# Kernel tuning notes

Measured on AMD Instinct MI355X. Metric: run time of the kernel, lower is better.

Reference implementation:

```python
import jax, jax.numpy as jnp
import numpy as np

N_SRC = 50000
N_DST = 50000
N_EDGES = 800000
D = 128
H = 128


def setup_inputs() -> dict:
    key = jax.random.key(0)
    ks = jax.random.split(key, 10)
    return {
        "feat_src": jax.random.normal(ks[0], (N_SRC, D), dtype=jnp.float32),
        "feat_dst": jax.random.normal(ks[1], (N_DST, D), dtype=jnp.float32),
        "W1": jax.random.normal(ks[2], (H, D), dtype=jnp.float32) * 0.05,
        "b1": jnp.zeros((H,), dtype=jnp.float32),
        "W2": jax.random.normal(ks[3], (H, 3 * D), dtype=jnp.float32) * 0.05,
        "b2": jnp.zeros((H,), dtype=jnp.float32),
        "W3": jax.random.normal(ks[4], (H, 2 * H), dtype=jnp.float32) * 0.05,
        "b3": jnp.zeros((H,), dtype=jnp.float32),
        "src_idx": jax.random.randint(ks[5], (N_EDGES,), 0, N_SRC, dtype=jnp.int32),
        "dst_idx": jax.random.randint(ks[6], (N_EDGES,), 0, N_DST, dtype=jnp.int32),
    }


def reference(feat_src, feat_dst, W1, b1, W2, b2, W3, b3, src_idx, dst_idx):
    n_dst = feat_dst.shape[0]
    # copy_u: gather source features along edges  [E, D]
    m = feat_src[src_idx]
    # fn.max -> 'max'; NOTE: source code's 'mean' is ALSO fn.max (faithful to bug)
    mx = jax.ops.segment_max(m, dst_idx, num_segments=n_dst)
    mx = jnp.where(jnp.isfinite(mx), mx, jnp.zeros_like(mx))  # zero-degree dst -> 0 (DGL convention)
    sm = jax.ops.segment_sum(m, dst_idx, num_segments=n_dst)
    agg = jnp.concatenate([mx, mx, sm], axis=1)  # [N_dst, 3D]
    z2 = agg @ W2.T + b2            # fc2
    z1 = feat_dst @ W1.T + b1       # fc1
    h = jax.nn.relu(jnp.concatenate([z2, z1], axis=1))  # [N_dst, 2H]
    out = jax.nn.relu(h @ W3.T + b3)  # fc3 = Linear + ReLU
    return out
```

## Files before the change

### kernel.cpp

```cpp
#include <hip/hip_runtime.h>
#include <math.h>

#define NDST 50000
#define NSRC 50000
#define NEDGE 800000
#define DF 128

#define NBUK 1563
#define NCH 128
#define EPC (NEDGE / NCH)
#define HN (NBUK * NCH)
#define CAP 1536

typedef __attribute__((ext_vector_type(4))) float f32x4;
typedef __attribute__((ext_vector_type(8))) short bf16x8;

__device__ __forceinline__ ushort f2bf(float f) {
    union { float f; unsigned int u; } c; c.f = f;
    unsigned int u = c.u;
    unsigned int r = (u + 0x7fffu + ((u >> 16) & 1u)) >> 16;
    return (ushort)r;
}
__device__ __forceinline__ float bflo(unsigned int u) {
    union { unsigned int u; float f; } c; c.u = u << 16; return c.f;
}
__device__ __forceinline__ float bfhi(unsigned int u) {
    union { unsigned int u; float f; } c; c.u = u & 0xffff0000u; return c.f;
}

#define PB_FS 1500
#define PB_FD 1500
#define PB_W 320
#define PB_Z 196
#define PB_TOT (PB_FS + PB_FD + PB_W + PB_Z)

__global__ void prep_all(const float* __restrict__ fs, unsigned int* __restrict__ fs_b,
                         const float* __restrict__ fd, unsigned int* __restrict__ fd_b,
                         uint4* __restrict__ hist4,
                         const float* __restrict__ W2, const float* __restrict__ W1,
                         const float* __restrict__ W3,
                         ushort* __restrict__ Wz_b, ushort* __restrict__ W1_b,
                         ushort* __restrict__ W3_b) {
    int b = blockIdx.x, tid = threadIdx.x;
    if (b < PB_FS + PB_FD) {
        const float* src = (b < PB_FS) ? fs : fd;
        unsigned int* dst = (b < PB_FS) ? fs_b : fd_b;
        int lb = (b < PB_FS) ? b : b - PB_FS;
        const int NU = NSRC * DF / 4;
        for (int u = lb * 256 + tid; u < NU; u += PB_FS * 256) {
            float4 v = ((const float4*)src)[u];
            unsigned int lo = (unsigned int)f2bf(v.x) | ((unsigned int)f2bf(v.y) << 16);
            unsigned int hi = (unsigned int)f2bf(v.z) | ((unsigned int)f2bf(v.w) << 16);
            ((uint2*)dst)[u] = make_uint2(lo, hi);
        }
    } else if (b < PB_FS + PB_FD + PB_W) {
        int i = (b - PB_FS - PB_FD) * 256 + tid;
        if (i < 128 * 256) {
            int c = i >> 8, k = i & 255;
            float v = (k < 128) ? (W2[c * 384 + k] + W2[c * 384 + 128 + k])
                                : W2[c * 384 + 128 + k];
            Wz_b[i] = f2bf(v);
        } else if (i < 128 * 256 + 128 * 128) {
            int j = i - 128 * 256;
            W1_b[j] = f2bf(W1[j]);
        } else if (i < 128 * 256 + 128 * 128 + 128 * 256) {
            int j = i - 128 * 256 - 128 * 128;
            W3_b[j] = f2bf(W3[j]);
        }
    } else {
        int i = (b - PB_FS - PB_FD - PB_W) * 256 + tid;
        if (i < HN / 4) hist4[i] = make_uint4(0, 0, 0, 0);
    }
}

__global__ void hist_k(const int* __restrict__ dst_idx, int* __restrict__ hist) {
    int c = blockIdx.x, tid = threadIdx.x;
    int base = c * EPC;
    for (int e = base + tid; e < base + EPC; e += 256)
        atomicAdd(&hist[(dst_idx[e] >> 5) * NCH + c], 1);
}

__global__ void scan_bsums(const int* __restrict__ a, int* __restrict__ bsum, int n) {
    __shared__ int ws[4];
    int i = blockIdx.x * 256 + threadIdx.x;
    int v = (i < n) ? a[i] : 0;
    #pragma unroll
    for (int off = 32; off > 0; off >>= 1) v += __shfl_down(v, off, 64);
    if ((threadIdx.x & 63) == 0) ws[threadIdx.x >> 6] = v;
    __syncthreads();
    if (threadIdx.x == 0) bsum[blockIdx.x] = ws[0] + ws[1] + ws[2] + ws[3];
}

__global__ __launch_bounds__(256)
void scan_mid(const int* __restrict__ bsum, int* __restrict__ bpre, int nb) {
    __shared__ int part[256];
    int t = threadIdx.x;
    int ch = (nb + 255) / 256;
    int lo = t * ch, hi = min(nb, lo + ch);
    int s = 0;
    for (int i = lo; i < hi; ++i) s += bsum[i];
    part[t] = s;
    __syncthreads();
    for (int off = 1; off < 256; off <<= 1) {
        int v = (t >= off) ? part[t - off] : 0;
        __syncthreads();
        part[t] += v;
        __syncthreads();
    }
    int run = (t == 0) ? 0 : part[t - 1];
    for (int i = lo; i < hi; ++i) { bpre[i] = run; run += bsum[i]; }
}

__global__ __launch_bounds__(256)
void scan_final(const int* __restrict__ a, const int* __restrict__ bpre,
                int* __restrict__ out, int n) {
    __shared__ int s[256];
    int b = blockIdx.x, t = threadIdx.x;
    int i = b * 256 + t;
    int v = (i < n) ? a[i] : 0;
    s[t] = v;
    __syncthreads();
    for (int off = 1; off < 256; off <<= 1) {
        int u = (t >= off) ? s[t - off] : 0;
        __syncthreads();
        s[t] += u;
        __syncthreads();
    }
    if (i < n) out[i] = bpre[b] + s[t] - v;
}

__global__ __launch_bounds__(256)
void partition_k(const int* __restrict__ src_idx, const int* __restrict__ dst_idx,
                 const int* __restrict__ scanned, unsigned int* __restrict__ pairs) {
    __shared__ int offs_l[NBUK];
    int c = blockIdx.x, tid = threadIdx.x;
    for (int i = tid; i < NBUK; i += 256) offs_l[i] = scanned[i * NCH + c];
    __syncthreads();
    int base = c * EPC;
    for (int e = base + tid; e < base + EPC; e += 256) {
        int d = dst_idx[e];
        int pos = atomicAdd(&offs_l[d >> 5], 1);
        pairs[pos] = (unsigned int)src_idx[e] | ((unsigned int)(d & 31) << 16);
    }
}

__global__ __launch_bounds__(256)
void bucket_sort_agg(const unsigned int* __restrict__ fs_b,
                     const unsigned int* __restrict__ pairs,
                     const int* __restrict__ scanned,
                     unsigned int* __restrict__ mx_b, unsigned int* __restrict__ sm_b) {
    __shared__ int s_src[CAP];
    __shared__ int s_cnt[32], s_off[32], s_cur[32];
    int B = blockIdx.x, tid = threadIdx.x;
    int w = tid >> 6, lane = tid & 63;
    int s0 = scanned[B * NCH];
    int s1 = (B + 1 < NBUK) ? scanned[(B + 1) * NCH] : NEDGE;

    float mx0[8], mx1[8], sm0[8], sm1[8];
    #pragma unroll
    for (int j = 0; j < 8; ++j) {
        mx0[j] = -INFINITY; mx1[j] = -INFINITY; sm0[j] = 0.f; sm1[j] = 0.f;
    }

    for (int cs = s0; cs < s1; cs += CAP) {
        int n = min(CAP, s1 - cs);
        if (tid < 32) s_cnt[tid] = 0;
        __syncthreads();
        for (int i = tid; i < n; i += 256)
            atomicAdd(&s_cnt[(pairs[cs + i] >> 16) & 31u], 1);
        __syncthreads();
        if (tid < 32) {
            int v = s_cnt[tid];
            int incl = v;
            #pragma unroll
            for (int d = 1; d < 32; d <<= 1) {
                int o = __shfl_up(incl, d, 64);
                if (tid >= d) incl += o;
            }
            s_off[tid] = incl - v;
            s_cur[tid] = incl - v;
        }
        __syncthreads();
        for (int i = tid; i < n; i += 256) {
            unsigned int p = pairs[cs + i];
            int pos = atomicAdd(&s_cur[(p >> 16) & 31u], 1);
            s_src[pos] = (int)(p & 0xFFFFu);
        }
        __syncthreads();
        #pragma unroll
        for (int j = 0; j < 8; ++j) {
            int dl = w * 8 + j;
            int e = s_off[dl], eend = e + s_cnt[dl];
            for (; e + 3 < eend; e += 4) {
                int i0 = s_src[e], i1 = s_src[e + 1], i2 = s_src[e + 2], i3 = s_src[e + 3];
                unsigned int u0 = fs_b[(size_t)i0 * 64 + lane];
                unsigned int u1 = fs_b[(size_t)i1 * 64 + lane];
                unsigned int u2 = fs_b[(size_t)i2 * 64 + lane];
                unsigned int u3 = fs_b[(size_t)i3 * 64 + lane];
                float a0 = bflo(u0), c0 = bfhi(u0);
                float a1 = bflo(u1), c1 = bfhi(u1);
                float a2 = bflo(u2), c2 = bfhi(u2);
                float a3 = bflo(u3), c3 = bfhi(u3);
                mx0[j] = fmaxf(fmaxf(fmaxf(mx0[j], a0), a1), fmaxf(a2, a3));
                mx1[j] = fmaxf(fmaxf(fmaxf(mx1[j], c0), c1), fmaxf(c2, c3));
                sm0[j] += (a0 + a1) + (a2 + a3);
                sm1[j] += (c0 + c1) + (c2 + c3);
            }
            for (; e < eend; ++e) {
                unsigned int u = fs_b[(size_t)s_src[e] * 64 + lane];
                float a = bflo(u), c = bfhi(u);
                mx0[j] = fmaxf(mx0[j], a);
                mx1[j] = fmaxf(mx1[j], c);
                sm0[j] += a;
                sm1[j] += c;
            }
        }
        __syncthreads();
    }

    int base_d = B * 32;
    #pragma unroll
    for (int j = 0; j < 8; ++j) {
        int d = base_d + w * 8 + j;
        if (d >= NDST) continue;
        float m0 = mx0[j], m1 = mx1[j];
        if (m0 == -INFINITY) m0 = 0.f;
        if (m1 == -INFINITY) m1 = 0.f;
        union { float f; unsigned int u; } c0, c1;
        c0.f = m0; c1.f = m1;
        size_t o = (size_t)d * 64 + lane;
        mx_b[o] = (c0.u >> 16) | (c1.u & 0xFFFF0000u);
        sm_b[o] = (unsigned int)f2bf(sm0[j]) | ((unsigned int)f2bf(sm1[j]) << 16);
    }
}

#define BM2 64
#define LDH 260
#define LDWS 40

__global__ __launch_bounds__(256)
void mlp_fused(const ushort* __restrict__ mxa, const ushort* __restrict__ sma,
               const ushort* __restrict__ fdb,
               const ushort* __restrict__ Wz_b, const ushort* __restrict__ W1_b,
               const ushort* __restrict__ W3_b,
               const float* __restrict__ b1, const float* __restrict__ b2,
               const float* __restrict__ b3,
               float* __restrict__ out) {
    __shared__ ushort Hs[BM2 * LDH];
    __shared__ ushort Ws[128 * LDWS];
    int tid = threadIdx.x;
    int bm = blockIdx.x * BM2;
    int wid = tid >> 6, lane = tid & 63;
    int wm = (wid & 1) * 32, wn = (wid >> 1) * 64;
    int lrow = lane & 15, lk8 = (lane >> 4) * 8;
    int rbase = (lane >> 4) * 4;

    int am0 = min(bm + wm + lrow, NDST - 1);
    int am1 = min(bm + wm + 16 + lrow, NDST - 1);
    int bn[4];
    #pragma unroll
    for (int ni = 0; ni < 4; ++ni) bn[ni] = wn + ni * 16 + lrow;

    int srw = tid >> 1, skw = (tid & 1) * 16;
    uint4 wr0, wr1;
    bf16x8 a0[2], a1[2];
    f32x4 acc[2][4];

#define STAGE_LOAD(Wb, K, k0) { const ushort* wp = (Wb) + (size_t)srw * (K) + (k0) + skw; \
                                wr0 = *(const uint4*)wp; wr1 = *(const uint4*)(wp + 8); }
#define STAGE_WRITE() { *(uint4*)&Ws[srw * LDWS + skw] = wr0; \
                        *(uint4*)&Ws[srw * LDWS + skw + 8] = wr1; }

    STAGE_LOAD(Wz_b, 256, 0);
    a0[0] = *(const bf16x8*)(mxa + (size_t)am0 * 128 + lk8);
    a1[0] = *(const bf16x8*)(mxa + (size_t)am1 * 128 + lk8);

    #pragma unroll
    for (int i = 0; i < 2; ++i)
        #pragma unroll
        for (int j = 0; j < 4; ++j) acc[i][j] = (f32x4){0.f, 0.f, 0.f, 0.f};
    #pragma unroll
    for (int k = 0; k < 8; ++k) {
        if (k) __syncthreads();
        STAGE_WRITE();
        __syncthreads();
        if (k < 7) { STAGE_LOAD(Wz_b, 256, (k + 1) * 32); }
        else       { STAGE_LOAD(W1_b, 128, 0); }
        if (k < 7) {
            const ushort* ap = (k + 1 < 4) ? mxa : sma;
            int kl = (((k + 1) * 32) & 127) + lk8;
            a0[(k + 1) & 1] = *(const bf16x8*)(ap + (size_t)am0 * 128 + kl);
            a1[(k + 1) & 1] = *(const bf16x8*)(ap + (size_t)am1 * 128 + kl);
        } else {
            a0[(k + 1) & 1] = *(const bf16x8*)(fdb + (size_t)am0 * 128 + lk8);
            a1[(k + 1) & 1] = *(const bf16x8*)(fdb + (size_t)am1 * 128 + lk8);
        }
        #pragma unroll
        for (int ni = 0; ni < 4; ++ni) {
            bf16x8 bf = *(const bf16x8*)&Ws[bn[ni] * LDWS + lk8];
            acc[0][ni] = __builtin_amdgcn_mfma_f32_16x16x32_bf16(a0[k & 1], bf, acc[0][ni], 0, 0, 0);
            acc[1][ni] = __builtin_amdgcn_mfma_f32_16x16x32_bf16(a1[k & 1], bf, acc[1][ni], 0, 0, 0);
        }
    }
    #pragma unroll
    for (int ni = 0; ni < 4; ++ni) {
        float bv = b2[bn[ni]];
        #pragma unroll
        for (int mi = 0; mi < 2; ++mi)
            #pragma unroll
            for (int r = 0; r < 4; ++r)
                Hs[(wm + mi * 16 + rbase + r) * LDH + bn[ni]] =
                    f2bf(fmaxf(acc[mi][ni][r] + bv, 0.f));
    }

    #pragma unroll
    for (int i = 0; i < 2; ++i)
        #pragma unroll
        for (int j = 0; j < 4; ++j) acc[i][j] = (f32x4){0.f, 0.f, 0.f, 0.f};
    #pragma unroll
    for (int k = 0; k < 4; ++k) {
        __syncthreads();
        STAGE_WRITE();
        __syncthreads();
        if (k < 3) { STAGE_LOAD(W1_b, 128, (k + 1) * 32); }
        else       { STAGE_LOAD(W3_b, 256, 0); }
        if (k < 3) {
            int kl = (k + 1) * 32 + lk8;
            a0[(k + 1) & 1] = *(const bf16x8*)(fdb + (size_t)am0 * 128 + kl);
            a1[(k + 1) & 1] = *(const bf16x8*)(fdb + (size_t)am1 * 128 + kl);
        }
        #pragma unroll
        for (int ni = 0; ni < 4; ++ni) {
            bf16x8 bf = *(const bf16x8*)&Ws[bn[ni] * LDWS + lk8];
            acc[0][ni] = __builtin_amdgcn_mfma_f32_16x16x32_bf16(a0[k & 1], bf, acc[0][ni], 0, 0, 0);
            acc[1][ni] = __builtin_amdgcn_mfma_f32_16x16x32_bf16(a1[k & 1], bf, acc[1][ni], 0, 0, 0);
        }
    }
    #pragma unroll
    for (int ni = 0; ni < 4; ++ni) {
        float bv = b1[bn[ni]];
        #pragma unroll
        for (int mi = 0; mi < 2; ++mi)
            #pragma unroll
            for (int r = 0; r < 4; ++r)
                Hs[(wm + mi * 16 + rbase + r) * LDH + 128 + bn[ni]] =
                    f2bf(fmaxf(acc[mi][ni][r] + bv, 0.f));
    }

    #pragma unroll
    for (int i = 0; i < 2; ++i)
        #pragma unroll
        for (int j = 0; j < 4; ++j) acc[i][j] = (f32x4){0.f, 0.f, 0.f, 0.f};
    #pragma unroll
    for (int k = 0; k < 8; ++k) {
        __syncthreads();
        STAGE_WRITE();
        __syncthreads();
        if (k < 7) { STAGE_LOAD(W3_b, 256, (k + 1) * 32); }
        bf16x8 af0 = *(const bf16x8*)&Hs[(wm + lrow) * LDH + k * 32 + lk8];
        bf16x8 af1 = *(const bf16x8*)&Hs[(wm + 16 + lrow) * LDH + k * 32 + lk8];
        #pragma unroll
        for (int ni = 0; ni < 4; ++ni) {
            bf16x8 bf = *(const bf16x8*)&Ws[bn[ni] * LDWS + lk8];
            acc[0][ni] = __builtin_amdgcn_mfma_f32_16x16x32_bf16(af0, bf, acc[0][ni], 0, 0, 0);
            acc[1][ni] = __builtin_amdgcn_mfma_f32_16x16x32_bf16(af1, bf, acc[1][ni], 0, 0, 0);
        }
    }
    #pragma unroll
    for (int ni = 0; ni < 4; ++ni) {
        float bv = b3[bn[ni]];
        #pragma unroll
        for (int mi = 0; mi < 2; ++mi)
            #pragma unroll
            for (int r = 0; r < 4; ++r) {
                int m = bm + wm + mi * 16 + rbase + r;
                if (m < NDST)
                    out[(size_t)m * 128 + bn[ni]] = fmaxf(acc[mi][ni][r] + bv, 0.f);
            }
    }
#undef STAGE_LOAD
#undef STAGE_WRITE
}

extern "C" void kernel_launch(void* const* d_in, const int* in_sizes, int n_in,
                              void* d_out, int out_size, void* d_ws, size_t ws_size,
                              hipStream_t stream) {
    const float* feat_src = (const float*)d_in[0];
    const float* feat_dst = (const float*)d_in[1];
    const float* W1 = (const float*)d_in[2];
    const float* b1 = (const float*)d_in[3];
    const float* W2 = (const float*)d_in[4];
    const float* b2 = (const float*)d_in[5];
    const float* W3 = (const float*)d_in[6];
    const float* b3 = (const float*)d_in[7];
    const int* src_idx = (const int*)d_in[8];
    const int* dst_idx = (const int*)d_in[9];

    float* out = (float*)d_out;

    unsigned int* fs_b = (unsigned int*)d_ws;
    unsigned int* mx_b = fs_b + (size_t)NSRC * 64;
    unsigned int* sm_b = mx_b + (size_t)NDST * 64;
    unsigned int* fd_b = sm_b + (size_t)NDST * 64;
    ushort* Wz_b = (ushort*)(fd_b + (size_t)NDST * 64);
    ushort* W1_b = Wz_b + 128 * 256;
    ushort* W3_b = W1_b + 128 * 128;
    int* hist    = (int*)(W3_b + 128 * 256);
    int* scanned = hist + HN;
    int* bsum    = scanned + HN;
    int* bpre    = bsum + 1024;
    unsigned int* pairs = (unsigned int*)(bpre + 1024);

    const int NBH = (HN + 255) / 256;

    prep_all<<<PB_TOT, 256, 0, stream>>>(
        feat_src, fs_b, feat_dst, fd_b, (uint4*)hist, W2, W1, W3, Wz_b, W1_b, W3_b);

    hist_k<<<NCH, 256, 0, stream>>>(dst_idx, hist);
    scan_bsums<<<NBH, 256, 0, stream>>>(hist, bsum, HN);
    scan_mid<<<1, 256, 0, stream>>>(bsum, bpre, NBH);
    scan_final<<<NBH, 256, 0, stream>>>(hist, bpre, scanned, HN);
    partition_k<<<NCH, 256, 0, stream>>>(src_idx, dst_idx, scanned, pairs);

    bucket_sort_agg<<<NBUK, 256, 0, stream>>>(fs_b, pairs, scanned, mx_b, sm_b);

    mlp_fused<<<(NDST + BM2 - 1) / BM2, 256, 0, stream>>>(
        (const ushort*)mx_b, (const ushort*)sm_b, (const ushort*)fd_b,
        Wz_b, W1_b, W3_b, b1, b2, b3, out);
}
```

Measured before the change: 149.8 us.

## Fuse feat_dst bf16 conversion into MLP kernel and unroll gather loop by eight

Drops the separate fp32-to-bf16 pass over feat_dst in the prep kernel. The MLP kernel now reads fp32 feat_dst directly and converts to bf16 in registers just before the MFMA, which removes one full write and re-read of a bf16 copy. The aggregation gather loop also gains an 8-wide unrolled stage to keep more independent loads in flight. The trade-off is twice the bytes per feat_dst load in the MLP and higher register pressure in both kernels.

```diff
diff --git a/kernel.cpp b/kernel.cpp
--- a/kernel.cpp
+++ b/kernel.cpp
@@ -27,34 +27,35 @@
 __device__ __forceinline__ float bfhi(unsigned int u) {
     union { unsigned int u; float f; } c; c.u = u & 0xffff0000u; return c.f;
 }
+__device__ __forceinline__ bf16x8 cvt8(float4 a, float4 b) {
+    union { bf16x8 v; ushort s[8]; } r;
+    r.s[0] = f2bf(a.x); r.s[1] = f2bf(a.y); r.s[2] = f2bf(a.z); r.s[3] = f2bf(a.w);
+    r.s[4] = f2bf(b.x); r.s[5] = f2bf(b.y); r.s[6] = f2bf(b.z); r.s[7] = f2bf(b.w);
+    return r.v;
+}
 
 #define PB_FS 1500
-#define PB_FD 1500
 #define PB_W 320
 #define PB_Z 196
-#define PB_TOT (PB_FS + PB_FD + PB_W + PB_Z)
+#define PB_TOT (PB_FS + PB_W + PB_Z)
 
 __global__ void prep_all(const float* __restrict__ fs, unsigned int* __restrict__ fs_b,
-                         const float* __restrict__ fd, unsigned int* __restrict__ fd_b,
                          uint4* __restrict__ hist4,
                          const float* __restrict__ W2, const float* __restrict__ W1,
                          const float* __restrict__ W3,
                          ushort* __restrict__ Wz_b, ushort* __restrict__ W1_b,
                          ushort* __restrict__ W3_b) {
     int b = blockIdx.x, tid = threadIdx.x;
-    if (b < PB_FS + PB_FD) {
-        const float* src = (b < PB_FS) ? fs : fd;
-        unsigned int* dst = (b < PB_FS) ? fs_b : fd_b;
-        int lb = (b < PB_FS) ? b : b - PB_FS;
+    if (b < PB_FS) {
         const int NU = NSRC * DF / 4;
-        for (int u = lb * 256 + tid; u < NU; u += PB_FS * 256) {
-            float4 v = ((const float4*)src)[u];
+        for (int u = b * 256 + tid; u < NU; u += PB_FS * 256) {
+            float4 v = ((const float4*)fs)[u];
             unsigned int lo = (unsigned int)f2bf(v.x) | ((unsigned int)f2bf(v.y) << 16);
             unsigned int hi = (unsigned int)f2bf(v.z) | ((unsigned int)f2bf(v.w) << 16);
-            ((uint2*)dst)[u] = make_uint2(lo, hi);
-        }
-    } else if (b < PB_FS + PB_FD + PB_W) {
-        int i = (b - PB_FS - PB_FD) * 256 + tid;
+            ((uint2*)fs_b)[u] = make_uint2(lo, hi);
+        }
+    } else if (b < PB_FS + PB_W) {
+        int i = (b - PB_FS) * 256 + tid;
         if (i < 128 * 256) {
             int c = i >> 8, k = i & 255;
             float v = (k < 128) ? (W2[c * 384 + k] + W2[c * 384 + 128 + k])
@@ -68,7 +69,7 @@
             W3_b[j] = f2bf(W3[j]);
         }
     } else {
-        int i = (b - PB_FS - PB_FD - PB_W) * 256 + tid;
+        int i = (b - PB_FS - PB_W) * 256 + tid;
         if (i < HN / 4) hist4[i] = make_uint4(0, 0, 0, 0);
     }
 }
@@ -191,12 +192,35 @@
         for (int j = 0; j < 8; ++j) {
             int dl = w * 8 + j;
             int e = s_off[dl], eend = e + s_cnt[dl];
+            for (; e + 7 < eend; e += 8) {
+                unsigned int u0 = fs_b[(size_t)s_src[e] * 64 + lane];
+                unsigned int u1 = fs_b[(size_t)s_src[e + 1] * 64 + lane];
+                unsigned int u2 = fs_b[(size_t)s_src[e + 2] * 64 + lane];
+                unsigned int u3 = fs_b[(size_t)s_src[e + 3] * 64 + lane];
+                unsigned int u4 = fs_b[(size_t)s_src[e + 4] * 64 + lane];
+                unsigned int u5 = fs_b[(size_t)s_src[e + 5] * 64 + lane];
+                unsigned int u6 = fs_b[(size_t)s_src[e + 6] * 64 + lane];
+                unsigned int u7 = fs_b[(size_t)s_src[e + 7] * 64 + lane];
+                float a0 = bflo(u0), c0 = bfhi(u0);
+                float a1 = bflo(u1), c1 = bfhi(u1);
+                float a2 = bflo(u2), c2 = bfhi(u2);
+                float a3 = bflo(u3), c3 = bfhi(u3);
+                float a4 = bflo(u4), c4 = bfhi(u4);
+                float a5 = bflo(u5), c5 = bfhi(u5);
+                float a6 = bflo(u6), c6 = bfhi(u6);
+                float a7 = bflo(u7), c7 = bfhi(u7);
+                mx0[j] = fmaxf(mx0[j], fmaxf(fmaxf(fmaxf(a0, a1), fmaxf(a2, a3)),
+                                             fmaxf(fmaxf(a4, a5), fmaxf(a6, a7))));
+                mx1[j] = fmaxf(mx1[j], fmaxf(fmaxf(fmaxf(c0, c1), fmaxf(c2, c3)),
+                                             fmaxf(fmaxf(c4, c5), fmaxf(c6, c7))));
+                sm0[j] += ((a0 + a1) + (a2 + a3)) + ((a4 + a5) + (a6 + a7));
+                sm1[j] += ((c0 + c1) + (c2 + c3)) + ((c4 + c5) + (c6 + c7));
+            }
             for (; e + 3 < eend; e += 4) {
-                int i0 = s_src[e], i1 = s_src[e + 1], i2 = s_src[e + 2], i3 = s_src[e + 3];
-                unsigned int u0 = fs_b[(size_t)i0 * 64 + lane];
-                unsigned int u1 = fs_b[(size_t)i1 * 64 + lane];
-                unsigned int u2 = fs_b[(size_t)i2 * 64 + lane];
-                unsigned int u3 = fs_b[(size_t)i3 * 64 + lane];
+                unsigned int u0 = fs_b[(size_t)s_src[e] * 64 + lane];
+                unsigned int u1 = fs_b[(size_t)s_src[e + 1] * 64 + lane];
+                unsigned int u2 = fs_b[(size_t)s_src[e + 2] * 64 + lane];
+                unsigned int u3 = fs_b[(size_t)s_src[e + 3] * 64 + lane];
                 float a0 = bflo(u0), c0 = bfhi(u0);
                 float a1 = bflo(u1), c1 = bfhi(u1);
                 float a2 = bflo(u2), c2 = bfhi(u2);
@@ -240,7 +264,7 @@
 
 __global__ __launch_bounds__(256)
 void mlp_fused(const ushort* __restrict__ mxa, const ushort* __restrict__ sma,
-               const ushort* __restrict__ fdb,
+               const float* __restrict__ fd,
                const ushort* __restrict__ Wz_b, const ushort* __restrict__ W1_b,
                const ushort* __restrict__ W3_b,
                const float* __restrict__ b1, const float* __restrict__ b2,
@@ -264,6 +288,7 @@
     int srw = tid >> 1, skw = (tid & 1) * 16;
     uint4 wr0, wr1;
     bf16x8 a0[2], a1[2];
+    float4 fa0[2][2], fa1[2][2];
     f32x4 acc[2][4];
 
 #define STAGE_LOAD(Wb, K, k0) { const ushort* wp = (Wb) + (size_t)srw * (K) + (k0) + skw; \
@@ -292,8 +317,10 @@
             a0[(k + 1) & 1] = *(const bf16x8*)(ap + (size_t)am0 * 128 + kl);
             a1[(k + 1) & 1] = *(const bf16x8*)(ap + (size_t)am1 * 128 + kl);
         } else {
-            a0[(k + 1) & 1] = *(const bf16x8*)(fdb + (size_t)am0 * 128 + lk8);
-            a1[(k + 1) & 1] = *(const bf16x8*)(fdb + (size_t)am1 * 128 + lk8);
+            const float* p0 = fd + (size_t)am0 * 128 + lk8;
+            const float* p1 = fd + (size_t)am1 * 128 + lk8;
+            fa0[0][0] = *(const float4*)p0; fa0[0][1] = *(const float4*)(p0 + 4);
+            fa1[0][0] = *(const float4*)p1; fa1[0][1] = *(const float4*)(p1 + 4);
         }
         #pragma unroll
         for (int ni = 0; ni < 4; ++ni) {
@@ -326,14 +353,20 @@
         else       { STAGE_LOAD(W3_b, 256, 0); }
         if (k < 3) {
             int kl = (k + 1) * 32 + lk8;
-            a0[(k + 1) & 1] = *(const bf16x8*)(fdb + (size_t)am0 * 128 + kl);
-            a1[(k + 1) & 1] = *(const bf16x8*)(fdb + (size_t)am1 * 128 + kl);
-        }
+            const float* p0 = fd + (size_t)am0 * 128 + kl;
+            const float* p1 = fd + (size_t)am1 * 128 + kl;
+            fa0[(k + 1) & 1][0] = *(const float4*)p0;
+            fa0[(k + 1) & 1][1] = *(const float4*)(p0 + 4);
+            fa1[(k + 1) & 1][0] = *(const float4*)p1;
+            fa1[(k + 1) & 1][1] = *(const float4*)(p1 + 4);
+        }
+        bf16x8 af0 = cvt8(fa0[k & 1][0], fa0[k & 1][1]);
+        bf16x8 af1 = cvt8(fa1[k & 1][0], fa1[k & 1][1]);
         #pragma unroll
         for (int ni = 0; ni < 4; ++ni) {
             bf16x8 bf = *(const bf16x8*)&Ws[bn[ni] * LDWS + lk8];
-            acc[0][ni] = __builtin_amdgcn_mfma_f32_16x16x32_bf16(a0[k & 1], bf, acc[0][ni], 0, 0, 0);
-            acc[1][ni] = __builtin_amdgcn_mfma_f32_16x16x32_bf16(a1[k & 1], bf, acc[1][ni], 0, 0, 0);
+            acc[0][ni] = __builtin_amdgcn_mfma_f32_16x16x32_bf16(af0, bf, acc[0][ni], 0, 0, 0);
+            acc[1][ni] = __builtin_amdgcn_mfma_f32_16x16x32_bf16(af1, bf, acc[1][ni], 0, 0, 0);
         }
     }
     #pragma unroll
@@ -401,8 +434,7 @@
     unsigned int* fs_b = (unsigned int*)d_ws;
     unsigned int* mx_b = fs_b + (size_t)NSRC * 64;
     unsigned int* sm_b = mx_b + (size_t)NDST * 64;
-    unsigned int* fd_b = sm_b + (size_t)NDST * 64;
-    ushort* Wz_b = (ushort*)(fd_b + (size_t)NDST * 64);
+    ushort* Wz_b = (ushort*)(sm_b + (size_t)NDST * 64);
     ushort* W1_b = Wz_b + 128 * 256;
     ushort* W3_b = W1_b + 128 * 128;
     int* hist    = (int*)(W3_b + 128 * 256);
@@ -414,7 +446,7 @@
     const int NBH = (HN + 255) / 256;
 
     prep_all<<<PB_TOT, 256, 0, stream>>>(
-        feat_src, fs_b, feat_dst, fd_b, (uint4*)hist, W2, W1, W3, Wz_b, W1_b, W3_b);
+        feat_src, fs_b, (uint4*)hist, W2, W1, W3, Wz_b, W1_b, W3_b);
 
     hist_k<<<NCH, 256, 0, stream>>>(dst_idx, hist);
     scan_bsums<<<NBH, 256, 0, stream>>>(hist, bsum, HN);
@@ -425,6 +457,6 @@
     bucket_sort_agg<<<NBUK, 256, 0, stream>>>(fs_b, pairs, scanned, mx_b, sm_b);
 
     mlp_fused<<<(NDST + BM2 - 1) / BM2, 256, 0, stream>>>(
-        (const ushort*)mx_b, (const ushort*)sm_b, (const ushort*)fd_b,
+        (const ushort*)mx_b, (const ushort*)sm_b, feat_dst,
         Wz_b, W1_b, W3_b, b1, b2, b3, out);
 }
```

Measured after the change: 146.4 us. 2.3% less time.
